# Optimization experiments

Measured on AMD Instinct MI355X. Metric: run time of the kernel, lower is better.

Reference implementation:

```python
import jax, jax.numpy as jnp
import numpy as np

# Module hyperparameters (from init_kwargs)
B, D = 512, 65536        # input: [B, D]
Q = 64                   # sub-vectors per sample
R = 8                    # number of independent KMeans problems
L = 64                   # clusters (codebook size) per problem
ITERS = 10               # KMeans max_iter
SUBD = D // Q            # sub-vector dim = 1024
N = B * Q // R           # points per KMeans problem = 4096


def setup_inputs() -> dict:
    key = jax.random.key(0)
    x = jax.random.normal(key, (B, D), dtype=jnp.float32)
    return {"x": x}


def _kmeans(pts):
    """Batched Lloyd's KMeans. pts: [R, N, d]. Returns (labels [R,N], centers [R,L,d])."""
    # init: random distinct points per group (torch_kmeans 'rnd' init)
    key = jax.random.key(42)
    init_idx = jax.vmap(lambda k: jax.random.permutation(k, N)[:L])(
        jax.random.split(key, R))                          # [R, L]
    centers = jax.vmap(lambda p, i: p[i])(pts, init_idx)   # [R, L, d]
    x2 = jnp.sum(pts * pts, axis=-1, keepdims=True)        # [R, N, 1]

    def assign(centers):
        c2 = jnp.sum(centers * centers, axis=-1)           # [R, L]
        d2 = x2 + c2[:, None, :] - 2.0 * jnp.einsum('rnd,rld->rnl', pts, centers)
        return jnp.argmin(d2, axis=-1)                     # [R, N]

    def step(centers, _):
        labels = assign(centers)
        onehot = jax.nn.one_hot(labels, L, dtype=pts.dtype)      # [R, N, L]
        counts = jnp.sum(onehot, axis=1)                          # [R, L]
        sums = jnp.einsum('rnl,rnd->rld', onehot, pts)            # [R, L, d]
        new_c = jnp.where(counts[..., None] > 0,
                          sums / jnp.maximum(counts[..., None], 1.0),
                          centers)                                # keep empty clusters
        return new_c, None

    centers, _ = jax.lax.scan(step, centers, None, length=ITERS)
    labels = assign(centers)
    return labels, centers


def _quantize(x):
    orig_shape = x.shape
    pts = x.reshape(B, Q, SUBD).reshape(R, N, SUBD)        # [R, N, d/q]
    labels, centers = _kmeans(pts)
    # gather: replace each point by its centroid
    xq = jax.vmap(lambda c, lab: c[lab])(centers, labels)  # [R, N, d/q]
    return xq.reshape(orig_shape)


def reference(x):
    # FedLite_Layer.forward in training mode
    return _quantize(x)
```

## Files before the change

kernel.cpp:

```cpp
#include <hip/hip_runtime.h>
#include <stdint.h>
#include <stddef.h>


#define JAX_PARTITIONABLE 1

static constexpr int R_    = 8;
static constexpr int N_    = 4096;
static constexpr int L_    = 64;
static constexpr int D_    = 1024;
static constexpr int ITERS = 10;
static constexpr int ROWS  = R_ * N_;
static constexpr int SEGS  = 8;

__device__ __forceinline__ unsigned rotl32(unsigned x, int r) {
  return (x << r) | (x >> (32 - r));
}

__device__ __forceinline__ void tf2x32(unsigned k0, unsigned k1,
                                       unsigned c0, unsigned c1,
                                       unsigned &o0, unsigned &o1) {
  unsigned ks2 = k0 ^ k1 ^ 0x1BD11BDAu;
  unsigned x0 = c0 + k0, x1 = c1 + k1;
#define TF_R4(a,b,c,d) { x0 += x1; x1 = rotl32(x1,a); x1 ^= x0; \
                         x0 += x1; x1 = rotl32(x1,b); x1 ^= x0; \
                         x0 += x1; x1 = rotl32(x1,c); x1 ^= x0; \
                         x0 += x1; x1 = rotl32(x1,d); x1 ^= x0; }
  TF_R4(13,15,26,6);  x0 += k1;  x1 += ks2 + 1u;
  TF_R4(17,29,16,24); x0 += ks2; x1 += k0  + 2u;
  TF_R4(13,15,26,6);  x0 += k0;  x1 += k1  + 3u;
  TF_R4(17,29,16,24); x0 += k1;  x1 += ks2 + 4u;
  TF_R4(13,15,26,6);  x0 += ks2; x1 += k0  + 5u;
#undef TF_R4
  o0 = x0; o1 = x1;
}

__device__ __forceinline__ void jax_split2(unsigned k0, unsigned k1,
                                           unsigned &nk0, unsigned &nk1,
                                           unsigned &sk0, unsigned &sk1) {
#if JAX_PARTITIONABLE
  tf2x32(k0, k1, 0u, 0u, nk0, nk1);
  tf2x32(k0, k1, 0u, 1u, sk0, sk1);
#else
  unsigned a0, a1, b0, b1;
  tf2x32(k0, k1, 0u, 2u, a0, a1);
  tf2x32(k0, k1, 1u, 3u, b0, b1);
  nk0 = a0; nk1 = b0; sk0 = a1; sk1 = b1;
#endif
}

__global__ __launch_bounds__(1024) void k_rng_x2(const float* __restrict__ pts,
                                                 float* __restrict__ x2,
                                                 int* __restrict__ init_idx) {
  __shared__ unsigned long long arr[N_];
  __shared__ unsigned short perm[N_];
  const int t = threadIdx.x;

  if (blockIdx.x >= R_) {
    const int row = (blockIdx.x - R_) * 16 + (t >> 6);
    const int lane = t & 63;
    const float4* P = (const float4*)(pts + (size_t)row * D_);
    float s = 0.f;
#pragma unroll
    for (int i = 0; i < 4; ++i) {
      float4 v = P[lane + 64 * i];
      s += v.x * v.x + v.y * v.y + v.z * v.z + v.w * v.w;
    }
#pragma unroll
    for (int m = 32; m > 0; m >>= 1) s += __shfl_down(s, m);
    if (lane == 0) x2[row] = s;
    return;
  }

  const int r = blockIdx.x;

  unsigned k0, k1;
#if JAX_PARTITIONABLE
  tf2x32(0u, 42u, 0u, (unsigned)r, k0, k1);
#else
  {
    unsigned a0, a1, b0, b1;
    unsigned i0 = 2u * r, i1 = 2u * r + 1u;
    if (r < 4) { tf2x32(0u, 42u, i0, i0 + 8u, a0, a1); tf2x32(0u, 42u, i1, i1 + 8u, b0, b1); k0 = a0; k1 = b0; }
    else       { tf2x32(0u, 42u, i0 - 8u, i0, a0, a1); tf2x32(0u, 42u, i1 - 8u, i1, b0, b1); k0 = a1; k1 = b1; }
  }
#endif

  for (int i = t; i < N_; i += 1024) perm[i] = (unsigned short)i;
  __syncthreads();

  for (int round = 0; round < 2; ++round) {
    unsigned nk0, nk1, sk0, sk1;
    jax_split2(k0, k1, nk0, nk1, sk0, sk1);
    for (int j = t; j < N_; j += 1024) {
      unsigned o0, o1, skey;
#if JAX_PARTITIONABLE
      tf2x32(sk0, sk1, 0u, (unsigned)j, o0, o1);
      skey = o0 ^ o1;
#else
      if (j < 2048) { tf2x32(sk0, sk1, (unsigned)j, (unsigned)(j + 2048), o0, o1); skey = o0; }
      else          { tf2x32(sk0, sk1, (unsigned)(j - 2048), (unsigned)j, o0, o1); skey = o1; }
#endif
      arr[j] = ((unsigned long long)skey << 24) |
               ((unsigned long long)(unsigned)j << 12) |
               (unsigned long long)perm[j];
    }
    __syncthreads();
    for (int k = 2; k <= N_; k <<= 1) {
      for (int j2 = k >> 1; j2 >= 1; j2 >>= 1) {
        for (int q = t; q < N_ / 2; q += 1024) {
          int low = q & (j2 - 1);
          int i0 = ((q ^ low) << 1) | low;
          int i1 = i0 | j2;
          bool up = ((i0 & k) == 0);
          unsigned long long a = arr[i0], b = arr[i1];
          if ((a > b) == up) { arr[i0] = b; arr[i1] = a; }
        }
        __syncthreads();
      }
    }
    for (int j = t; j < N_; j += 1024) perm[j] = (unsigned short)(arr[j] & 0xFFFull);
    __syncthreads();
    k0 = nk0; k1 = nk1;
  }
  if (t < L_) init_idx[r * L_ + t] = (int)perm[t];
}

__global__ __launch_bounds__(256) void k_gather_init(const float* __restrict__ pts,
                                                     const int* __restrict__ init_idx,
                                                     float* __restrict__ centers,
                                                     float* __restrict__ c2,
                                                     int* __restrict__ counts) {
  const int l = blockIdx.x, r = blockIdx.y, t = threadIdx.x;
  const int idx = init_idx[r * L_ + l];
  const float4* src = (const float4*)(pts + ((size_t)r * N_ + idx) * D_);
  float4* dst = (float4*)(centers + ((size_t)r * L_ + l) * D_);
  float4 v = src[t];
  dst[t] = v;
  float s = v.x * v.x + v.y * v.y + v.z * v.z + v.w * v.w;
  __shared__ float red[4];
  const int lane = t & 63, wave = t >> 6;
#pragma unroll
  for (int m = 32; m > 0; m >>= 1) s += __shfl_down(s, m);
  if (lane == 0) red[wave] = s;
  __syncthreads();
  if (t == 0) {
    c2[r * L_ + l] = red[0] + red[1] + red[2] + red[3];
    counts[r * L_ + l] = 0;
  }
}

#define BN 128
#define BK 64
__global__ __launch_bounds__(256, 1) void k_assign(const float* __restrict__ pts,
                                                   const float* __restrict__ centers,
                                                   const float* __restrict__ c2g,
                                                   const float* __restrict__ x2g,
                                                   int* __restrict__ labels,
                                                   int* __restrict__ counts) {
  __shared__ __align__(16) float pT[2][BK][BN + 4];
  __shared__ __align__(16) float cT[2][BK][L_ + 4];
  __shared__ int hist[L_];
  const int t = threadIdx.x;
  const int r = blockIdx.y;
  const int n0 = blockIdx.x * BN;
  const int pg = t >> 3;
  const int cg = t & 7;
  const int p0 = pg * 4;
  const int l0 = cg * 8;

  const float* Pr = pts + ((size_t)r * N_ + n0) * D_;
  const float* Cr = centers + (size_t)r * L_ * D_;

  const int srow = t >> 4;
  const int skk  = (t & 15) * 4;

  if (t < L_) hist[t] = 0;

  float4 pv[8], cv[4];

#pragma unroll
  for (int i = 0; i < 8; ++i)
    pv[i] = *(const float4*)(Pr + (size_t)(i * 16 + srow) * D_ + skk);
#pragma unroll
  for (int i = 0; i < 4; ++i)
    cv[i] = *(const float4*)(Cr + (size_t)(i * 16 + srow) * D_ + skk);
#pragma unroll
  for (int i = 0; i < 8; ++i) {
    const int p = i * 16 + srow;
    pT[0][skk + 0][p] = pv[i].x; pT[0][skk + 1][p] = pv[i].y;
    pT[0][skk + 2][p] = pv[i].z; pT[0][skk + 3][p] = pv[i].w;
  }
#pragma unroll
  for (int i = 0; i < 4; ++i) {
    const int l = i * 16 + srow;
    cT[0][skk + 0][l] = cv[i].x; cT[0][skk + 1][l] = cv[i].y;
    cT[0][skk + 2][l] = cv[i].z; cT[0][skk + 3][l] = cv[i].w;
  }
  __syncthreads();

  float acc[4][8];
#pragma unroll
  for (int i = 0; i < 4; ++i)
#pragma unroll
    for (int j = 0; j < 8; ++j) acc[i][j] = 0.f;

  constexpr int NKB = D_ / BK;
  for (int kb = 0; kb < NKB; ++kb) {
    const int cur = kb & 1;
    if (kb + 1 < NKB) {
      const int kbase = (kb + 1) * BK;
#pragma unroll
      for (int i = 0; i < 8; ++i)
        pv[i] = *(const float4*)(Pr + (size_t)(i * 16 + srow) * D_ + kbase + skk);
#pragma unroll
      for (int i = 0; i < 4; ++i)
        cv[i] = *(const float4*)(Cr + (size_t)(i * 16 + srow) * D_ + kbase + skk);
    }

    for (int kk = 0; kk < BK; ++kk) {
      float4 pvv = *(const float4*)&pT[cur][kk][p0];
      float4 ca  = *(const float4*)&cT[cur][kk][l0];
      float4 cb  = *(const float4*)&cT[cur][kk][l0 + 4];
      float pvs[4] = {pvv.x, pvv.y, pvv.z, pvv.w};
      float cvs[8] = {ca.x, ca.y, ca.z, ca.w, cb.x, cb.y, cb.z, cb.w};
#pragma unroll
      for (int i = 0; i < 4; ++i)
#pragma unroll
        for (int j = 0; j < 8; ++j)
          acc[i][j] = fmaf(pvs[i], cvs[j], acc[i][j]);
    }

    if (kb + 1 < NKB) {
      const int nxt = cur ^ 1;
#pragma unroll
      for (int i = 0; i < 8; ++i) {
        const int p = i * 16 + srow;
        pT[nxt][skk + 0][p] = pv[i].x; pT[nxt][skk + 1][p] = pv[i].y;
        pT[nxt][skk + 2][p] = pv[i].z; pT[nxt][skk + 3][p] = pv[i].w;
      }
#pragma unroll
      for (int i = 0; i < 4; ++i) {
        const int l = i * 16 + srow;
        cT[nxt][skk + 0][l] = cv[i].x; cT[nxt][skk + 1][l] = cv[i].y;
        cT[nxt][skk + 2][l] = cv[i].z; cT[nxt][skk + 3][l] = cv[i].w;
      }
    }
    __syncthreads();
  }

  float c2v[8];
#pragma unroll
  for (int j = 0; j < 8; ++j) c2v[j] = c2g[r * L_ + l0 + j];

#pragma unroll
  for (int i = 0; i < 4; ++i) {
    const int n = n0 + p0 + i;
    const float x2i = x2g[r * N_ + n];
    float bv = 3.4e38f;
    int bi = 0;
#pragma unroll
    for (int j = 0; j < 8; ++j) {
      float d2 = (x2i + c2v[j]) - 2.0f * acc[i][j];
      if (d2 < bv) { bv = d2; bi = l0 + j; }
    }
#pragma unroll
    for (int m = 1; m < 8; m <<= 1) {
      float ov = __shfl_xor(bv, m);
      int oi = __shfl_xor(bi, m);
      if (ov < bv || (ov == bv && oi < bi)) { bv = ov; bi = oi; }
    }
    if (cg == 0) {
      labels[r * N_ + n] = bi;
      atomicAdd(&hist[bi], 1);
    }
  }
  __syncthreads();
  if (t < L_) atomicAdd(&counts[r * L_ + t], hist[t]);
}

__global__ __launch_bounds__(256) void k_update(const float* __restrict__ pts,
                                                const int* __restrict__ labels,
                                                float* __restrict__ psums) {
  __shared__ float acc[L_ * 256];
  __shared__ int lab[512];
  const int dch = blockIdx.x;
  const int seg = blockIdx.y;
  const int r   = blockIdx.z;
  const int t = threadIdx.x;

  for (int i = t; i < L_ * 256; i += 256) acc[i] = 0.f;
  for (int i = t; i < 512; i += 256) lab[i] = labels[r * N_ + seg * 512 + i];
  __syncthreads();

  const float* P = pts + ((size_t)r * N_ + seg * 512) * D_ + dch * 256 + t;
#pragma unroll 4
  for (int n = 0; n < 512; ++n) {
    int l = lab[n];
    acc[l * 256 + t] += P[(size_t)n * D_];
  }
  __syncthreads();

  float* S = psums + (((size_t)r * SEGS + seg) * L_) * D_ + dch * 256;
  for (int i = t; i < L_ * 256; i += 256) {
    int l = i >> 8, dd = i & 255;
    S[(size_t)l * D_ + dd] = acc[i];
  }
}

__global__ __launch_bounds__(256) void k_reduce(const float* __restrict__ psums,
                                                int* __restrict__ counts,
                                                float* __restrict__ centers,
                                                float* __restrict__ c2) {
  const int l = blockIdx.x, r = blockIdx.y, t = threadIdx.x;
  const int cnt = counts[r * L_ + l];
  const float denom = fmaxf((float)cnt, 1.0f);

  float4 s = {0.f, 0.f, 0.f, 0.f};
#pragma unroll
  for (int seg = 0; seg < SEGS; ++seg) {
    const float4 v = *(const float4*)(psums + (((size_t)r * SEGS + seg) * L_ + l) * D_ + t * 4);
    s.x += v.x; s.y += v.y; s.z += v.z; s.w += v.w;
  }
  float4* Crow = (float4*)(centers + ((size_t)r * L_ + l) * D_);
  float4 cn;
  if (cnt > 0) {
    cn.x = s.x / denom; cn.y = s.y / denom; cn.z = s.z / denom; cn.w = s.w / denom;
  } else {
    cn = Crow[t];
  }
  Crow[t] = cn;

  float ssq = cn.x * cn.x + cn.y * cn.y + cn.z * cn.z + cn.w * cn.w;
  __shared__ float red[4];
  const int lane = t & 63, wave = t >> 6;
#pragma unroll
  for (int m = 32; m > 0; m >>= 1) ssq += __shfl_down(ssq, m);
  if (lane == 0) red[wave] = ssq;
  __syncthreads();
  if (t == 0) {
    c2[r * L_ + l] = red[0] + red[1] + red[2] + red[3];
    counts[r * L_ + l] = 0;
  }
}

__global__ __launch_bounds__(256) void k_final(const float* __restrict__ centers,
                                               const int* __restrict__ labels,
                                               float* __restrict__ out) {
  const int t = threadIdx.x;
  const int row = blockIdx.x * 4 + (t >> 6);
  const int lane = t & 63;
  const int r = row >> 12;
  const int lab = labels[row];
  const float4* src = (const float4*)(centers + ((size_t)r * L_ + lab) * D_);
  float4* dst = (float4*)(out + (size_t)row * D_);
#pragma unroll
  for (int i = 0; i < 4; ++i) dst[lane + 64 * i] = src[lane + 64 * i];
}

extern "C" void kernel_launch(void* const* d_in, const int* in_sizes, int n_in,
                              void* d_out, int out_size, void* d_ws, size_t ws_size,
                              hipStream_t stream) {
  const float* x = (const float*)d_in[0];
  float* out = (float*)d_out;
  char* ws = (char*)d_ws;

  float* centers = (float*)(ws + 0);
  float* c2      = (float*)(ws + 2097152);
  float* x2      = (float*)(ws + 2099200);
  int*   labels  = (int*)  (ws + 2230272);
  int*   counts  = (int*)  (ws + 2361344);
  int*   initidx = (int*)  (ws + 2363392);
  float* psums   = (float*)(ws + 2365440);
  (void)in_sizes; (void)n_in; (void)out_size; (void)ws_size;

  k_rng_x2<<<dim3(R_ + ROWS / 16), 1024, 0, stream>>>(x, x2, initidx);
  k_gather_init<<<dim3(L_, R_), 256, 0, stream>>>(x, initidx, centers, c2, counts);

  for (int it = 0; it < ITERS; ++it) {
    k_assign<<<dim3(N_ / BN, R_), 256, 0, stream>>>(x, centers, c2, x2, labels, counts);
    k_update<<<dim3(4, SEGS, R_), 256, 0, stream>>>(x, labels, psums);
    k_reduce<<<dim3(L_, R_), 256, 0, stream>>>(psums, counts, centers, c2);
  }
  k_assign<<<dim3(N_ / BN, R_), 256, 0, stream>>>(x, centers, c2, x2, labels, counts);
  k_final<<<dim3(ROWS / 4), 256, 0, stream>>>(centers, labels, out);
}
```

Before: 1.807 ms.

## Store transposed centers and read them directly per wave in assign

Adds a transposed [R][D][L] copy of the centers, written in gather_init and reduce, so k_assign can read each wave's 16-center slice straight from global/L2 (wave-uniform addresses) instead of staging centers through shared memory. Each lane now owns two points and the argmin is combined across waves through shared memory. The point tile in LDS gets an XOR swizzle to reduce bank conflicts. k_update is also software-pipelined with an 8-deep register prefetch of point rows. The risk is that per-k scalar/global loads of centers in the inner loop are more latency-bound than LDS reads, and the transposed stores are strided.

```diff
diff --git a/kernel.cpp b/kernel.cpp
--- a/kernel.cpp
+++ b/kernel.cpp
@@ -129,6 +129,7 @@
 __global__ __launch_bounds__(256) void k_gather_init(const float* __restrict__ pts,
                                                      const int* __restrict__ init_idx,
                                                      float* __restrict__ centers,
+                                                     float* __restrict__ centersT,
                                                      float* __restrict__ c2,
                                                      int* __restrict__ counts) {
   const int l = blockIdx.x, r = blockIdx.y, t = threadIdx.x;
@@ -137,6 +138,13 @@
   float4* dst = (float4*)(centers + ((size_t)r * L_ + l) * D_);
   float4 v = src[t];
   dst[t] = v;
+  {
+    const int k0 = t * 4;
+    centersT[((size_t)r * D_ + k0 + 0) * L_ + l] = v.x;
+    centersT[((size_t)r * D_ + k0 + 1) * L_ + l] = v.y;
+    centersT[((size_t)r * D_ + k0 + 2) * L_ + l] = v.z;
+    centersT[((size_t)r * D_ + k0 + 3) * L_ + l] = v.w;
+  }
   float s = v.x * v.x + v.y * v.y + v.z * v.z + v.w * v.w;
   __shared__ float red[4];
   const int lane = t & 63, wave = t >> 6;
@@ -153,57 +161,50 @@
 #define BN 128
 #define BK 64
 __global__ __launch_bounds__(256, 1) void k_assign(const float* __restrict__ pts,
-                                                   const float* __restrict__ centers,
+                                                   const float* __restrict__ centersT,
                                                    const float* __restrict__ c2g,
                                                    const float* __restrict__ x2g,
                                                    int* __restrict__ labels,
                                                    int* __restrict__ counts) {
   __shared__ __align__(16) float pT[2][BK][BN + 4];
-  __shared__ __align__(16) float cT[2][BK][L_ + 4];
-  __shared__ int hist[L_];
+  __shared__ float smv[4][BN];
+  __shared__ int   smi[4][BN];
+  __shared__ int   hist[L_];
   const int t = threadIdx.x;
   const int r = blockIdx.y;
   const int n0 = blockIdx.x * BN;
-  const int pg = t >> 3;
-  const int cg = t & 7;
-  const int p0 = pg * 4;
-  const int l0 = cg * 8;
+  const int lane = t & 63;
+  const int wv = __builtin_amdgcn_readfirstlane(t >> 6);
 
   const float* Pr = pts + ((size_t)r * N_ + n0) * D_;
-  const float* Cr = centers + (size_t)r * L_ * D_;
+  const float* Cw = centersT + (size_t)r * D_ * L_ + wv * 16;
 
   const int srow = t >> 4;
-  const int skk  = (t & 15) * 4;
+  const int q    = t & 15;
+  const int skk  = q * 4;
+  const int swz  = 4 * (q & 7);
 
   if (t < L_) hist[t] = 0;
 
-  float4 pv[8], cv[4];
-
+  float4 pv4[8];
 #pragma unroll
   for (int i = 0; i < 8; ++i)
-    pv[i] = *(const float4*)(Pr + (size_t)(i * 16 + srow) * D_ + skk);
-#pragma unroll
-  for (int i = 0; i < 4; ++i)
-    cv[i] = *(const float4*)(Cr + (size_t)(i * 16 + srow) * D_ + skk);
+    pv4[i] = *(const float4*)(Pr + (size_t)(i * 16 + srow) * D_ + skk);
 #pragma unroll
   for (int i = 0; i < 8; ++i) {
-    const int p = i * 16 + srow;
-    pT[0][skk + 0][p] = pv[i].x; pT[0][skk + 1][p] = pv[i].y;
-    pT[0][skk + 2][p] = pv[i].z; pT[0][skk + 3][p] = pv[i].w;
-  }
-#pragma unroll
-  for (int i = 0; i < 4; ++i) {
-    const int l = i * 16 + srow;
-    cT[0][skk + 0][l] = cv[i].x; cT[0][skk + 1][l] = cv[i].y;
-    cT[0][skk + 2][l] = cv[i].z; cT[0][skk + 3][l] = cv[i].w;
-  }
-  __syncthreads();
-
-  float acc[4][8];
-#pragma unroll
-  for (int i = 0; i < 4; ++i)
-#pragma unroll
-    for (int j = 0; j < 8; ++j) acc[i][j] = 0.f;
+    const int col = (i * 16 + srow) ^ swz;
+    pT[0][skk + 0][col] = pv4[i].x;
+    pT[0][skk + 1][col] = pv4[i].y;
+    pT[0][skk + 2][col] = pv4[i].z;
+    pT[0][skk + 3][col] = pv4[i].w;
+  }
+  __syncthreads();
+
+  float acc[2][16];
+#pragma unroll
+  for (int ip = 0; ip < 2; ++ip)
+#pragma unroll
+    for (int j = 0; j < 16; ++j) acc[ip][j] = 0.f;
 
   constexpr int NKB = D_ / BK;
   for (int kb = 0; kb < NKB; ++kb) {
@@ -212,68 +213,70 @@
       const int kbase = (kb + 1) * BK;
 #pragma unroll
       for (int i = 0; i < 8; ++i)
-        pv[i] = *(const float4*)(Pr + (size_t)(i * 16 + srow) * D_ + kbase + skk);
-#pragma unroll
-      for (int i = 0; i < 4; ++i)
-        cv[i] = *(const float4*)(Cr + (size_t)(i * 16 + srow) * D_ + kbase + skk);
-    }
-
+        pv4[i] = *(const float4*)(Pr + (size_t)(i * 16 + srow) * D_ + kbase + skk);
+    }
+
+    const float* Ck = Cw + (size_t)kb * BK * L_;
+#pragma unroll 4
     for (int kk = 0; kk < BK; ++kk) {
-      float4 pvv = *(const float4*)&pT[cur][kk][p0];
-      float4 ca  = *(const float4*)&cT[cur][kk][l0];
-      float4 cb  = *(const float4*)&cT[cur][kk][l0 + 4];
-      float pvs[4] = {pvv.x, pvv.y, pvv.z, pvv.w};
-      float cvs[8] = {ca.x, ca.y, ca.z, ca.w, cb.x, cb.y, cb.z, cb.w};
-#pragma unroll
-      for (int i = 0; i < 4; ++i)
-#pragma unroll
-        for (int j = 0; j < 8; ++j)
-          acc[i][j] = fmaf(pvs[i], cvs[j], acc[i][j]);
+      const float* ck = Ck + kk * L_;
+      float cv[16];
+#pragma unroll
+      for (int j = 0; j < 16; ++j) cv[j] = ck[j];
+      const int colp = (2 * lane) ^ (4 * ((kk >> 2) & 7));
+      const float2 pp = *(const float2*)&pT[cur][kk][colp];
+#pragma unroll
+      for (int j = 0; j < 16; ++j) {
+        acc[0][j] = fmaf(pp.x, cv[j], acc[0][j]);
+        acc[1][j] = fmaf(pp.y, cv[j], acc[1][j]);
+      }
     }
 
     if (kb + 1 < NKB) {
       const int nxt = cur ^ 1;
 #pragma unroll
       for (int i = 0; i < 8; ++i) {
-        const int p = i * 16 + srow;
-        pT[nxt][skk + 0][p] = pv[i].x; pT[nxt][skk + 1][p] = pv[i].y;
-        pT[nxt][skk + 2][p] = pv[i].z; pT[nxt][skk + 3][p] = pv[i].w;
+        const int col = (i * 16 + srow) ^ swz;
+        pT[nxt][skk + 0][col] = pv4[i].x;
+        pT[nxt][skk + 1][col] = pv4[i].y;
+        pT[nxt][skk + 2][col] = pv4[i].z;
+        pT[nxt][skk + 3][col] = pv4[i].w;
       }
-#pragma unroll
-      for (int i = 0; i < 4; ++i) {
-        const int l = i * 16 + srow;
-        cT[nxt][skk + 0][l] = cv[i].x; cT[nxt][skk + 1][l] = cv[i].y;
-        cT[nxt][skk + 2][l] = cv[i].z; cT[nxt][skk + 3][l] = cv[i].w;
-      }
     }
     __syncthreads();
   }
 
-  float c2v[8];
-#pragma unroll
-  for (int j = 0; j < 8; ++j) c2v[j] = c2g[r * L_ + l0 + j];
-
-#pragma unroll
-  for (int i = 0; i < 4; ++i) {
-    const int n = n0 + p0 + i;
+  float c2v[16];
+#pragma unroll
+  for (int j = 0; j < 16; ++j) c2v[j] = c2g[r * L_ + wv * 16 + j];
+
+#pragma unroll
+  for (int ip = 0; ip < 2; ++ip) {
+    const int pl = lane * 2 + ip;
+    const int n = n0 + pl;
     const float x2i = x2g[r * N_ + n];
     float bv = 3.4e38f;
     int bi = 0;
 #pragma unroll
-    for (int j = 0; j < 8; ++j) {
-      float d2 = (x2i + c2v[j]) - 2.0f * acc[i][j];
-      if (d2 < bv) { bv = d2; bi = l0 + j; }
-    }
-#pragma unroll
-    for (int m = 1; m < 8; m <<= 1) {
-      float ov = __shfl_xor(bv, m);
-      int oi = __shfl_xor(bi, m);
-      if (ov < bv || (ov == bv && oi < bi)) { bv = ov; bi = oi; }
-    }
-    if (cg == 0) {
-      labels[r * N_ + n] = bi;
-      atomicAdd(&hist[bi], 1);
-    }
+    for (int j = 0; j < 16; ++j) {
+      float d2 = (x2i + c2v[j]) - 2.0f * acc[ip][j];
+      if (d2 < bv) { bv = d2; bi = wv * 16 + j; }
+    }
+    smv[wv][pl] = bv;
+    smi[wv][pl] = bi;
+  }
+  __syncthreads();
+  if (t < BN) {
+    float bv = smv[0][t];
+    int bi = smi[0][t];
+#pragma unroll
+    for (int w = 1; w < 4; ++w) {
+      float ov = smv[w][t];
+      int oi = smi[w][t];
+      if (ov < bv) { bv = ov; bi = oi; }
+    }
+    labels[r * N_ + n0 + t] = bi;
+    atomicAdd(&hist[bi], 1);
   }
   __syncthreads();
   if (t < L_) atomicAdd(&counts[r * L_ + t], hist[t]);
@@ -294,11 +297,20 @@
   __syncthreads();
 
   const float* P = pts + ((size_t)r * N_ + seg * 512) * D_ + dch * 256 + t;
-#pragma unroll 4
-  for (int n = 0; n < 512; ++n) {
-    int l = lab[n];
-    acc[l * 256 + t] += P[(size_t)n * D_];
-  }
+  float vbuf[8];
+#pragma unroll
+  for (int w = 0; w < 8; ++w) vbuf[w] = P[(size_t)w * D_];
+  for (int nb = 0; nb < 504; nb += 8) {
+#pragma unroll
+    for (int w = 0; w < 8; ++w) {
+      const int n = nb + w;
+      const float cur = vbuf[w];
+      vbuf[w] = P[(size_t)(n + 8) * D_];
+      acc[lab[n] * 256 + t] += cur;
+    }
+  }
+#pragma unroll
+  for (int w = 0; w < 8; ++w) acc[lab[504 + w] * 256 + t] += vbuf[w];
   __syncthreads();
 
   float* S = psums + (((size_t)r * SEGS + seg) * L_) * D_ + dch * 256;
@@ -311,6 +323,7 @@
 __global__ __launch_bounds__(256) void k_reduce(const float* __restrict__ psums,
                                                 int* __restrict__ counts,
                                                 float* __restrict__ centers,
+                                                float* __restrict__ centersT,
                                                 float* __restrict__ c2) {
   const int l = blockIdx.x, r = blockIdx.y, t = threadIdx.x;
   const int cnt = counts[r * L_ + l];
@@ -330,6 +343,13 @@
     cn = Crow[t];
   }
   Crow[t] = cn;
+  {
+    const int k0 = t * 4;
+    centersT[((size_t)r * D_ + k0 + 0) * L_ + l] = cn.x;
+    centersT[((size_t)r * D_ + k0 + 1) * L_ + l] = cn.y;
+    centersT[((size_t)r * D_ + k0 + 2) * L_ + l] = cn.z;
+    centersT[((size_t)r * D_ + k0 + 3) * L_ + l] = cn.w;
+  }
 
   float ssq = cn.x * cn.x + cn.y * cn.y + cn.z * cn.z + cn.w * cn.w;
   __shared__ float red[4];
@@ -365,23 +385,24 @@
   float* out = (float*)d_out;
   char* ws = (char*)d_ws;
 
-  float* centers = (float*)(ws + 0);
-  float* c2      = (float*)(ws + 2097152);
-  float* x2      = (float*)(ws + 2099200);
-  int*   labels  = (int*)  (ws + 2230272);
-  int*   counts  = (int*)  (ws + 2361344);
-  int*   initidx = (int*)  (ws + 2363392);
-  float* psums   = (float*)(ws + 2365440);
+  float* centers  = (float*)(ws + 0);
+  float* c2       = (float*)(ws + 2097152);
+  float* x2       = (float*)(ws + 2099200);
+  int*   labels   = (int*)  (ws + 2230272);
+  int*   counts   = (int*)  (ws + 2361344);
+  int*   initidx  = (int*)  (ws + 2363392);
+  float* psums    = (float*)(ws + 2365440);
+  float* centersT = (float*)(ws + 19142656);
   (void)in_sizes; (void)n_in; (void)out_size; (void)ws_size;
 
   k_rng_x2<<<dim3(R_ + ROWS / 16), 1024, 0, stream>>>(x, x2, initidx);
-  k_gather_init<<<dim3(L_, R_), 256, 0, stream>>>(x, initidx, centers, c2, counts);
+  k_gather_init<<<dim3(L_, R_), 256, 0, stream>>>(x, initidx, centers, centersT, c2, counts);
 
   for (int it = 0; it < ITERS; ++it) {
-    k_assign<<<dim3(N_ / BN, R_), 256, 0, stream>>>(x, centers, c2, x2, labels, counts);
+    k_assign<<<dim3(N_ / BN, R_), 256, 0, stream>>>(x, centersT, c2, x2, labels, counts);
     k_update<<<dim3(4, SEGS, R_), 256, 0, stream>>>(x, labels, psums);
-    k_reduce<<<dim3(L_, R_), 256, 0, stream>>>(psums, counts, centers, c2);
-  }
-  k_assign<<<dim3(N_ / BN, R_), 256, 0, stream>>>(x, centers, c2, x2, labels, counts);
+    k_reduce<<<dim3(L_, R_), 256, 0, stream>>>(psums, counts, centers, centersT, c2);
+  }
+  k_assign<<<dim3(N_ / BN, R_), 256, 0, stream>>>(x, centersT, c2, x2, labels, counts);
   k_final<<<dim3(ROWS / 4), 256, 0, stream>>>(centers, labels, out);
 }
```

Measured after the change: 2.040 ms. 12.9% more time.

## Retile assign GEMM with swizzled LDS, DPP center broadcast, and prefetch update loads

Applied to the files above, without the earlier changes.

The assign kernel's register tile is reorganised so each thread covers 8 points by 4 centers. Center values are loaded row-major into LDS and broadcast across lane quads with DPP moves. The transposed point tile uses an XOR swizzle to avoid LDS bank conflicts, and the argmin reduction now shuffles across the quad groups. Separately, the update kernel prefetches 8 rows ahead in registers so global load latency overlaps the shared-memory scatter-add, at the cost of more registers and more complex indexing.

```diff
diff --git a/kernel.cpp b/kernel.cpp
--- a/kernel.cpp
+++ b/kernel.cpp
@@ -159,51 +159,55 @@
                                                    int* __restrict__ labels,
                                                    int* __restrict__ counts) {
   __shared__ __align__(16) float pT[2][BK][BN + 4];
-  __shared__ __align__(16) float cT[2][BK][L_ + 4];
+  __shared__ __align__(16) float cL[2][L_][BK + 4];
   __shared__ int hist[L_];
   const int t = threadIdx.x;
   const int r = blockIdx.y;
   const int n0 = blockIdx.x * BN;
-  const int pg = t >> 3;
-  const int cg = t & 7;
-  const int p0 = pg * 4;
-  const int l0 = cg * 8;
+  const int lane = t & 63;
+  const int w  = t >> 6;
+  const int u  = lane & 3;
+  const int qq = lane >> 2;
+  const int p0 = (w * 4 + u) * 8;
+  const int l0 = qq * 4;
 
   const float* Pr = pts + ((size_t)r * N_ + n0) * D_;
   const float* Cr = centers + (size_t)r * L_ * D_;
 
   const int srow = t >> 4;
   const int skk  = (t & 15) * 4;
+  const int swz  = 4 * (t & 7);
+  const int crow = t >> 2;
+  const int cseg = (t & 3) * 16;
 
   if (t < L_) hist[t] = 0;
 
-  float4 pv[8], cv[4];
+  float4 pv4[8], cv4[4];
 
 #pragma unroll
   for (int i = 0; i < 8; ++i)
-    pv[i] = *(const float4*)(Pr + (size_t)(i * 16 + srow) * D_ + skk);
-#pragma unroll
-  for (int i = 0; i < 4; ++i)
-    cv[i] = *(const float4*)(Cr + (size_t)(i * 16 + srow) * D_ + skk);
+    pv4[i] = *(const float4*)(Pr + (size_t)(i * 16 + srow) * D_ + skk);
+#pragma unroll
+  for (int c = 0; c < 4; ++c)
+    cv4[c] = *(const float4*)(Cr + (size_t)crow * D_ + cseg + 4 * c);
 #pragma unroll
   for (int i = 0; i < 8; ++i) {
-    const int p = i * 16 + srow;
-    pT[0][skk + 0][p] = pv[i].x; pT[0][skk + 1][p] = pv[i].y;
-    pT[0][skk + 2][p] = pv[i].z; pT[0][skk + 3][p] = pv[i].w;
-  }
-#pragma unroll
-  for (int i = 0; i < 4; ++i) {
-    const int l = i * 16 + srow;
-    cT[0][skk + 0][l] = cv[i].x; cT[0][skk + 1][l] = cv[i].y;
-    cT[0][skk + 2][l] = cv[i].z; cT[0][skk + 3][l] = cv[i].w;
-  }
-  __syncthreads();
-
-  float acc[4][8];
-#pragma unroll
-  for (int i = 0; i < 4; ++i)
-#pragma unroll
-    for (int j = 0; j < 8; ++j) acc[i][j] = 0.f;
+    const int col = (i * 16 + srow) ^ swz;
+    pT[0][skk + 0][col] = pv4[i].x;
+    pT[0][skk + 1][col] = pv4[i].y;
+    pT[0][skk + 2][col] = pv4[i].z;
+    pT[0][skk + 3][col] = pv4[i].w;
+  }
+#pragma unroll
+  for (int c = 0; c < 4; ++c)
+    *(float4*)&cL[0][crow][cseg + 4 * c] = cv4[c];
+  __syncthreads();
+
+  float acc[8][4];
+#pragma unroll
+  for (int i = 0; i < 8; ++i)
+#pragma unroll
+    for (int j = 0; j < 4; ++j) acc[i][j] = 0.f;
 
   constexpr int NKB = D_ / BK;
   for (int kb = 0; kb < NKB; ++kb) {
@@ -212,65 +216,78 @@
       const int kbase = (kb + 1) * BK;
 #pragma unroll
       for (int i = 0; i < 8; ++i)
-        pv[i] = *(const float4*)(Pr + (size_t)(i * 16 + srow) * D_ + kbase + skk);
-#pragma unroll
-      for (int i = 0; i < 4; ++i)
-        cv[i] = *(const float4*)(Cr + (size_t)(i * 16 + srow) * D_ + kbase + skk);
-    }
-
-    for (int kk = 0; kk < BK; ++kk) {
-      float4 pvv = *(const float4*)&pT[cur][kk][p0];
-      float4 ca  = *(const float4*)&cT[cur][kk][l0];
-      float4 cb  = *(const float4*)&cT[cur][kk][l0 + 4];
-      float pvs[4] = {pvv.x, pvv.y, pvv.z, pvv.w};
-      float cvs[8] = {ca.x, ca.y, ca.z, ca.w, cb.x, cb.y, cb.z, cb.w};
-#pragma unroll
-      for (int i = 0; i < 4; ++i)
-#pragma unroll
-        for (int j = 0; j < 8; ++j)
-          acc[i][j] = fmaf(pvs[i], cvs[j], acc[i][j]);
+        pv4[i] = *(const float4*)(Pr + (size_t)(i * 16 + srow) * D_ + kbase + skk);
+#pragma unroll
+      for (int c = 0; c < 4; ++c)
+        cv4[c] = *(const float4*)(Cr + (size_t)crow * D_ + kbase + cseg + 4 * c);
+    }
+
+#pragma unroll 4
+    for (int kk4 = 0; kk4 < 16; ++kk4) {
+      const int sig4 = 4 * (kk4 & 7);
+      const int colA = p0 ^ sig4;
+      const float4 cq = *(const float4*)&cL[cur][lane][kk4 * 4];
+      const float ca[4] = {cq.x, cq.y, cq.z, cq.w};
+#pragma unroll
+      for (int e = 0; e < 4; ++e) {
+        const int kk = kk4 * 4 + e;
+        const float4 A = *(const float4*)&pT[cur][kk][colA];
+        const float4 B = *(const float4*)&pT[cur][kk][colA ^ 4];
+        const int ci = __float_as_int(ca[e]);
+        const float cb0 = __int_as_float(__builtin_amdgcn_mov_dpp(ci, 0x00, 0xF, 0xF, true));
+        const float cb1 = __int_as_float(__builtin_amdgcn_mov_dpp(ci, 0x55, 0xF, 0xF, true));
+        const float cb2 = __int_as_float(__builtin_amdgcn_mov_dpp(ci, 0xAA, 0xF, 0xF, true));
+        const float cb3 = __int_as_float(__builtin_amdgcn_mov_dpp(ci, 0xFF, 0xF, 0xF, true));
+        const float pv[8] = {A.x, A.y, A.z, A.w, B.x, B.y, B.z, B.w};
+#pragma unroll
+        for (int i = 0; i < 8; ++i) {
+          acc[i][0] = fmaf(pv[i], cb0, acc[i][0]);
+          acc[i][1] = fmaf(pv[i], cb1, acc[i][1]);
+          acc[i][2] = fmaf(pv[i], cb2, acc[i][2]);
+          acc[i][3] = fmaf(pv[i], cb3, acc[i][3]);
+        }
+      }
     }
 
     if (kb + 1 < NKB) {
       const int nxt = cur ^ 1;
 #pragma unroll
       for (int i = 0; i < 8; ++i) {
-        const int p = i * 16 + srow;
-        pT[nxt][skk + 0][p] = pv[i].x; pT[nxt][skk + 1][p] = pv[i].y;
-        pT[nxt][skk + 2][p] = pv[i].z; pT[nxt][skk + 3][p] = pv[i].w;
+        const int col = (i * 16 + srow) ^ swz;
+        pT[nxt][skk + 0][col] = pv4[i].x;
+        pT[nxt][skk + 1][col] = pv4[i].y;
+        pT[nxt][skk + 2][col] = pv4[i].z;
+        pT[nxt][skk + 3][col] = pv4[i].w;
       }
 #pragma unroll
-      for (int i = 0; i < 4; ++i) {
-        const int l = i * 16 + srow;
-        cT[nxt][skk + 0][l] = cv[i].x; cT[nxt][skk + 1][l] = cv[i].y;
-        cT[nxt][skk + 2][l] = cv[i].z; cT[nxt][skk + 3][l] = cv[i].w;
-      }
+      for (int c = 0; c < 4; ++c)
+        *(float4*)&cL[nxt][crow][cseg + 4 * c] = cv4[c];
     }
     __syncthreads();
   }
 
-  float c2v[8];
-#pragma unroll
-  for (int j = 0; j < 8; ++j) c2v[j] = c2g[r * L_ + l0 + j];
-
-#pragma unroll
-  for (int i = 0; i < 4; ++i) {
+  float c2v[4];
+#pragma unroll
+  for (int j = 0; j < 4; ++j) c2v[j] = c2g[r * L_ + l0 + j];
+
+#pragma unroll
+  for (int i = 0; i < 8; ++i) {
     const int n = n0 + p0 + i;
     const float x2i = x2g[r * N_ + n];
     float bv = 3.4e38f;
     int bi = 0;
 #pragma unroll
-    for (int j = 0; j < 8; ++j) {
+    for (int j = 0; j < 4; ++j) {
       float d2 = (x2i + c2v[j]) - 2.0f * acc[i][j];
       if (d2 < bv) { bv = d2; bi = l0 + j; }
     }
 #pragma unroll
-    for (int m = 1; m < 8; m <<= 1) {
+    for (int m = 4; m <= 32; m <<= 1) {
       float ov = __shfl_xor(bv, m);
       int oi = __shfl_xor(bi, m);
       if (ov < bv || (ov == bv && oi < bi)) { bv = ov; bi = oi; }
     }
-    if (cg == 0) {
+    if (qq == 0) {
       labels[r * N_ + n] = bi;
       atomicAdd(&hist[bi], 1);
     }
@@ -294,11 +311,20 @@
   __syncthreads();
 
   const float* P = pts + ((size_t)r * N_ + seg * 512) * D_ + dch * 256 + t;
-#pragma unroll 4
-  for (int n = 0; n < 512; ++n) {
-    int l = lab[n];
-    acc[l * 256 + t] += P[(size_t)n * D_];
-  }
+  float vbuf[8];
+#pragma unroll
+  for (int w = 0; w < 8; ++w) vbuf[w] = P[(size_t)w * D_];
+  for (int nb = 0; nb < 504; nb += 8) {
+#pragma unroll
+    for (int w = 0; w < 8; ++w) {
+      const int n = nb + w;
+      const float cur = vbuf[w];
+      vbuf[w] = P[(size_t)(n + 8) * D_];
+      acc[lab[n] * 256 + t] += cur;
+    }
+  }
+#pragma unroll
+  for (int w = 0; w < 8; ++w) acc[lab[504 + w] * 256 + t] += vbuf[w];
   __syncthreads();
 
   float* S = psums + (((size_t)r * SEGS + seg) * L_) * D_ + dch * 256;
```

Result: no change. 1.786 ms (-1.2%).
